# Kernel optimization log

Measured on AMD Instinct MI355X. Metric: run time of the kernel, lower is better.

The kernel has to match this reference:

```python
import jax, jax.numpy as jnp
import numpy as np

N_NODES = 50000


def _gcn_conv(x, edge_index, W, b):
    # x: [N, F_in], edge_index: [2, E] (with self-loops already added)
    n = x.shape[0]
    src, dst = edge_index[0], edge_index[1]
    h = x @ W  # [N, F_out] transform first (as in PyG GCNConv)
    deg = jax.ops.segment_sum(jnp.ones_like(dst, dtype=h.dtype), dst, num_segments=n)
    dinv = jax.lax.rsqrt(jnp.maximum(deg, 1.0))  # self-loops guarantee deg >= 1
    norm = dinv[src] * dinv[dst]  # [E]
    msg = h[src] * norm[:, None]  # [E, F_out] gather + scale
    out = jax.ops.segment_sum(msg, dst, num_segments=n)  # scatter-add to targets
    return out + b


def setup_inputs() -> dict:
    key = jax.random.key(0)
    k1, k2, k3, k4 = jax.random.split(key, 4)
    num_features, hidden, num_classes = 128, 128, 16
    n, e = N_NODES, 800000
    x = jax.random.normal(k1, (n, num_features), dtype=jnp.float32)
    edge_index = jax.random.randint(k2, (2, e), 0, n, dtype=jnp.int64)
    # add self-loops (PyG GCNConv default add_self_loops=True)
    loops = jnp.arange(n, dtype=jnp.int64)
    edge_index = jnp.concatenate([edge_index, jnp.stack([loops, loops])], axis=1)
    s1 = 1.0 / np.sqrt(num_features)
    s2 = 1.0 / np.sqrt(hidden)
    W1 = jax.random.uniform(k3, (num_features, hidden), jnp.float32, -s1, s1)
    b1 = jnp.zeros((hidden,), jnp.float32)
    W2 = jax.random.uniform(k4, (hidden, num_classes), jnp.float32, -s2, s2)
    b2 = jnp.zeros((num_classes,), jnp.float32)
    return {"x": x, "edge_index": edge_index, "W1": W1, "b1": b1, "W2": W2, "b2": b2}


def reference(x, edge_index, W1, b1, W2, b2):
    h = jax.nn.relu(_gcn_conv(x, edge_index, W1, b1))
    # dropout is identity in eval mode (deterministic reference)
    h = _gcn_conv(h, edge_index, W2, b2)
    return jax.nn.log_softmax(h, axis=1)
```

## Files before the change

kernel.cpp:

```cpp
#include <hip/hip_runtime.h>


typedef unsigned int uint32;
typedef unsigned short u16;
typedef __attribute__((ext_vector_type(8))) short bf16x8;
typedef __attribute__((ext_vector_type(4))) float f32x4;

#define NBMAX 1024
#define CHUNK 4096
#define EH 8192

__device__ inline u16 bf16rn(float f) {
    unsigned u = __float_as_uint(f);
    return (u16)((u + 0x7fffu + ((u >> 16) & 1u)) >> 16);
}

__device__ inline void bffma(float2& a, float w, uint32 u) {
    a.x = fmaf(w, __uint_as_float(u << 16), a.x);
    a.y = fmaf(w, __uint_as_float(u & 0xffff0000u), a.y);
}

__global__ __launch_bounds__(256) void k_combo(
    const float* __restrict__ x, const float* __restrict__ W1,
    const int* __restrict__ dstv, int* __restrict__ gh,
    u16* __restrict__ h, int N, int E, int NB, int ntile)
{
    __shared__ __align__(16) unsigned char smem[128 * 136 * 2];
    int t = threadIdx.x;

    if ((int)blockIdx.x >= ntile) {
        int* hl = (int*)smem;
        int hb = blockIdx.x - ntile;
        int e0 = hb * EH, e1 = min(e0 + EH, E);
        for (int i = t; i < NB; i += 256) hl[i] = 0;
        __syncthreads();
        for (int e = e0 + t; e < e1; e += 256)
            atomicAdd(&hl[dstv[e] >> 8], 1);
        __syncthreads();
        for (int i = t; i < NB; i += 256) {
            int c = hl[i];
            if (c) atomicAdd(&gh[i], c);
        }
        return;
    }

    u16* Wl = (u16*)smem;
    const float4* Wg4 = (const float4*)W1;
    for (int g = t; g < 128 * 32; g += 256) {
        int k = g >> 5, n4 = (g & 31) * 4;
        float4 v = Wg4[g];
        Wl[(n4 + 0) * 136 + k] = bf16rn(v.x);
        Wl[(n4 + 1) * 136 + k] = bf16rn(v.y);
        Wl[(n4 + 2) * 136 + k] = bf16rn(v.z);
        Wl[(n4 + 3) * 136 + k] = bf16rn(v.w);
    }
    __syncthreads();

    int wave = t >> 6, lane = t & 63;
    int quad = lane >> 4, ln = lane & 15;
    int rowbase = blockIdx.x * 64 + wave * 16;
    int node = rowbase + ln;
    int rclamp = min(node, N - 1);

    f32x4 acc[8];
    #pragma unroll
    for (int ct = 0; ct < 8; ++ct) acc[ct] = (f32x4){0.f, 0.f, 0.f, 0.f};

    #pragma unroll
    for (int q = 0; q < 4; ++q) {
        const float4* xr = (const float4*)(x + (size_t)rclamp * 128 + q * 32 + quad * 8);
        float4 a0 = xr[0], a1 = xr[1];
        bf16x8 xfr;
        xfr[0] = (short)bf16rn(a0.x); xfr[1] = (short)bf16rn(a0.y);
        xfr[2] = (short)bf16rn(a0.z); xfr[3] = (short)bf16rn(a0.w);
        xfr[4] = (short)bf16rn(a1.x); xfr[5] = (short)bf16rn(a1.y);
        xfr[6] = (short)bf16rn(a1.z); xfr[7] = (short)bf16rn(a1.w);
        #pragma unroll
        for (int ct = 0; ct < 8; ++ct) {
            bf16x8 wfr = *(const bf16x8*)&Wl[(ct * 16 + ln) * 136 + q * 32 + quad * 8];
            acc[ct] = __builtin_amdgcn_mfma_f32_16x16x32_bf16(wfr, xfr, acc[ct], 0, 0, 0);
        }
    }
    if (node < N) {
        u16* hp = h + (size_t)node * 128 + quad * 4;
        #pragma unroll
        for (int ct = 0; ct < 8; ++ct) {
            uint2 v;
            v.x = (uint32)bf16rn(acc[ct][0]) | ((uint32)bf16rn(acc[ct][1]) << 16);
            v.y = (uint32)bf16rn(acc[ct][2]) | ((uint32)bf16rn(acc[ct][3]) << 16);
            *(uint2*)(hp + ct * 16) = v;
        }
    }
}

__global__ __launch_bounds__(1024) void k_scanB(
    const int* __restrict__ gh, int* __restrict__ bbase,
    int* __restrict__ bfill, int NB, int E)
{
    __shared__ int s[1024];
    int t = threadIdx.x;
    int v = (t < NB) ? gh[t] : 0;
    s[t] = v;
    __syncthreads();
    for (int off = 1; off < 1024; off <<= 1) {
        int u = (t >= off) ? s[t - off] : 0;
        __syncthreads();
        s[t] += u;
        __syncthreads();
    }
    if (t < NB) {
        bbase[t] = s[t] - v;
        bfill[t] = 0;
    }
    if (t == 0) bbase[NB] = E;
}

__global__ __launch_bounds__(512) void k_partition(
    const int* __restrict__ src, const int* __restrict__ dstv,
    const int* __restrict__ bbase, int* __restrict__ bfill,
    uint32* __restrict__ tmp, int E, int NB)
{
    __shared__ int cntL[NBMAX];
    __shared__ int baseL[NBMAX];
    int t = threadIdx.x;
    int e0 = blockIdx.x * CHUNK;
    int e1 = min(e0 + CHUNK, E);
    for (int i = t; i < NB; i += 512) cntL[i] = 0;
    __syncthreads();
    for (int e = e0 + t; e < e1; e += 512)
        atomicAdd(&cntL[dstv[e] >> 8], 1);
    __syncthreads();
    for (int i = t; i < NB; i += 512) {
        int cc = cntL[i];
        baseL[i] = cc ? bbase[i] + atomicAdd(&bfill[i], cc) : 0;
        cntL[i] = 0;
    }
    __syncthreads();
    for (int e = e0 + t; e < e1; e += 512) {
        int sv = src[e], d = dstv[e];
        int b = d >> 8;
        int r = atomicAdd(&cntL[b], 1);
        tmp[baseL[b] + r] = (uint32)sv | ((uint32)(d & 255) << 16);
    }
}

__global__ __launch_bounds__(512) void k_bsort(
    const uint32* __restrict__ tmp, const int* __restrict__ bbase,
    u16* __restrict__ ssrc, int* __restrict__ rs,
    float* __restrict__ dinv, int N)
{
    __shared__ int cnt[256];
    __shared__ int ofs[256];
    int t = threadIdx.x;
    int b = blockIdx.x;
    int base = bbase[b];
    int endb = bbase[b + 1];
    int node0 = b << 8;

    if (t < 256) cnt[t] = 0;
    __syncthreads();
    for (int i = base + t; i < endb; i += 512)
        atomicAdd(&cnt[(tmp[i] >> 16) & 255], 1);
    __syncthreads();
    int v = (t < 256) ? cnt[t] : 0;
    __syncthreads();
    for (int off = 1; off < 256; off <<= 1) {
        int u = (t >= off && t < 256) ? cnt[t - off] : 0;
        __syncthreads();
        if (t < 256) cnt[t] += u;
        __syncthreads();
    }
    if (t < 256) {
        int node = node0 + t;
        if (node < N) {
            dinv[node] = rsqrtf(fmaxf((float)v, 1.0f));
            rs[node] = base + cnt[t];
        }
        ofs[t] = base + cnt[t] - v;
    }
    __syncthreads();
    for (int i = base + t; i < endb; i += 512) {
        uint32 rec = tmp[i];
        int pos = atomicAdd(&ofs[(rec >> 16) & 255], 1);
        ssrc[pos] = (u16)(rec & 0xffffu);
    }
}

__global__ __launch_bounds__(256) void k_pullg(
    const int* __restrict__ rs, const u16* __restrict__ ssrc,
    const float* __restrict__ dinv, const uint2* __restrict__ h,
    const float* __restrict__ b1, const float* __restrict__ W2,
    u16* __restrict__ h2, int N)
{
    __shared__ float W2T[16 * 132];
    __shared__ float rowbuf[8 * 132];
    int t = threadIdx.x;

    for (int g = t; g < 2048; g += 256) {
        int k = g >> 4, f = g & 15;
        W2T[f * 132 + k] = W2[g];
    }

    int wave = t >> 6, lane = t & 63;
    int sub = lane >> 5;
    int rl = lane & 31;
    int rowbase = blockIdx.x * 8;
    int n = rowbase + wave * 2 + sub;
    bool valid = (n < N);
    int nc = valid ? n : 0;
    int start = valid ? ((nc == 0) ? 0 : rs[nc - 1]) : 0;
    int len   = valid ? (rs[nc] - start) : 0;
    float dn  = valid ? dinv[nc] : 0.f;
    int lenMax = max(len, __shfl_xor(len, 32));

    float2 aA[4], aB[4];
    #pragma unroll
    for (int k = 0; k < 4; ++k) {
        aA[k] = (float2){0.f, 0.f};
        aB[k] = (float2){0.f, 0.f};
    }

    for (int tt = 0; tt < lenMax; tt += 4) {
        int s[4];
        uint2 u[4];
        float w[4];
        #pragma unroll
        for (int k = 0; k < 4; ++k) {
            bool act = (tt + k) < len;
            int jj = act ? (start + tt + k) : 0;
            s[k] = (int)ssrc[jj];
            w[k] = act ? 1.f : 0.f;
        }
        #pragma unroll
        for (int k = 0; k < 4; ++k)
            u[k] = h[(size_t)s[k] * 32 + rl];
        #pragma unroll
        for (int k = 0; k < 4; ++k)
            w[k] *= dn * dinv[s[k]];
        #pragma unroll
        for (int k = 0; k < 4; ++k) {
            bffma(aA[k], w[k], u[k].x);
            bffma(aB[k], w[k], u[k].y);
        }
    }

    {
        int r = wave * 2 + sub;
        float4 bb = ((const float4*)b1)[rl];
        float4 v;
        v.x = fmaxf(((aA[0].x + aA[1].x) + (aA[2].x + aA[3].x)) + bb.x, 0.f);
        v.y = fmaxf(((aA[0].y + aA[1].y) + (aA[2].y + aA[3].y)) + bb.y, 0.f);
        v.z = fmaxf(((aB[0].x + aB[1].x) + (aB[2].x + aB[3].x)) + bb.z, 0.f);
        v.w = fmaxf(((aB[0].y + aB[1].y) + (aB[2].y + aB[3].y)) + bb.w, 0.f);
        ((float4*)rowbuf)[r * 33 + rl] = v;
    }
    __syncthreads();

    if (t < 128) {
        int f = t & 15, r = t >> 4;
        const float4* W4 = (const float4*)W2T;
        const float4* rb4 = (const float4*)rowbuf;
        float acc = 0.f;
        #pragma unroll 8
        for (int k4 = 0; k4 < 32; ++k4) {
            float4 w = W4[f * 33 + k4];
            float4 xv = rb4[r * 33 + k4];
            acc = fmaf(xv.x, w.x, acc);
            acc = fmaf(xv.y, w.y, acc);
            acc = fmaf(xv.z, w.z, acc);
            acc = fmaf(xv.w, w.w, acc);
        }
        int rn = rowbase + r;
        if (rn < N) h2[(size_t)rn * 16 + f] = bf16rn(acc);
    }
}

__global__ __launch_bounds__(256) void k_pull2(
    const int* __restrict__ rs, const u16* __restrict__ ssrc,
    const float* __restrict__ dinv, const uint32* __restrict__ h2,
    const float* __restrict__ b2, float* __restrict__ out, int N)
{
    int idx = blockIdx.x * 256 + threadIdx.x;
    int n = idx >> 3;
    if (n >= N) return;
    int c = idx & 7;
    int start = (n == 0) ? 0 : rs[n - 1];
    int len = rs[n] - start;
    float dn = dinv[n];

    float2 a[4];
    #pragma unroll
    for (int k = 0; k < 4; ++k) a[k] = (float2){0.f, 0.f};

    for (int tt = 0; tt < len; tt += 4) {
        int s[4];
        uint32 u[4];
        float w[4];
        #pragma unroll
        for (int k = 0; k < 4; ++k) {
            bool act = (tt + k) < len;
            int jj = act ? (start + tt + k) : 0;
            s[k] = (int)ssrc[jj];
            w[k] = act ? 1.f : 0.f;
        }
        #pragma unroll
        for (int k = 0; k < 4; ++k)
            u[k] = h2[(size_t)s[k] * 8 + c];
        #pragma unroll
        for (int k = 0; k < 4; ++k)
            w[k] *= dn * dinv[s[k]];
        #pragma unroll
        for (int k = 0; k < 4; ++k)
            bffma(a[k], w[k], u[k]);
    }

    float acc0 = (a[0].x + a[1].x) + (a[2].x + a[3].x);
    float acc1 = (a[0].y + a[1].y) + (a[2].y + a[3].y);
    float v0 = acc0 + b2[2 * c];
    float v1 = acc1 + b2[2 * c + 1];
    float m = fmaxf(v0, v1);
    #pragma unroll
    for (int off = 1; off < 8; off <<= 1) m = fmaxf(m, __shfl_xor(m, off));
    float s = expf(v0 - m) + expf(v1 - m);
    #pragma unroll
    for (int off = 1; off < 8; off <<= 1) s += __shfl_xor(s, off);
    float ls = logf(s);
    float2 r = {v0 - m - ls, v1 - m - ls};
    ((float2*)out)[(size_t)n * 8 + c] = r;
}

extern "C" void kernel_launch(void* const* d_in, const int* in_sizes, int n_in,
                              void* d_out, int out_size, void* d_ws, size_t ws_size,
                              hipStream_t stream) {
    const float* x  = (const float*)d_in[0];
    const int*   ei = (const int*)d_in[1];
    const float* W1 = (const float*)d_in[2];
    const float* b1 = (const float*)d_in[3];
    const float* W2 = (const float*)d_in[4];
    const float* b2 = (const float*)d_in[5];
    float* outp = (float*)d_out;

    const int E = in_sizes[1] / 2;
    const int N = in_sizes[0] / 128;
    const int NB = (N + 255) >> 8;
    const int NH = (E + EH - 1) / EH;
    const int ntile = (N + 63) / 64;
    const int* src  = ei;
    const int* dstv = ei + E;

    const int Npad = (N + 255) & ~255;
    const int Epad = (E + 255) & ~255;
    int*   gh    = (int*)d_ws;
    int*   bbase = gh + NBMAX;
    int*   bfill = bbase + NBMAX + 256;
    int*   rs    = bfill + NBMAX;
    float* dinv  = (float*)(rs + Npad);
    uint32* tmp  = (uint32*)(dinv + Npad);
    u16*   ssrc  = (u16*)(tmp + Epad);
    uintptr_t hp = ((uintptr_t)(ssrc + Epad) + 255) & ~(uintptr_t)255;
    u16*   h     = (u16*)hp;
    u16*   h2    = h + (size_t)Npad * 128;

    hipMemsetAsync(gh, 0, NBMAX * sizeof(int), stream);
    k_combo<<<ntile + NH, 256, 0, stream>>>(x, W1, dstv, gh, h, N, E, NB, ntile);
    k_scanB<<<1, 1024, 0, stream>>>(gh, bbase, bfill, NB, E);
    k_partition<<<(E + CHUNK - 1) / CHUNK, 512, 0, stream>>>(src, dstv, bbase,
                                                             bfill, tmp, E, NB);
    k_bsort<<<NB, 512, 0, stream>>>(tmp, bbase, ssrc, rs, dinv, N);
    k_pullg<<<(N + 7) / 8, 256, 0, stream>>>(rs, ssrc, dinv, (const uint2*)h,
                                             b1, W2, h2, N);
    k_pull2<<<(N * 8 + 255) / 256, 256, 0, stream>>>(rs, ssrc, dinv,
                                                     (const uint32*)h2, b2, outp, N);
}
```

Baseline: 172.1 us.

## Tune partition/bsort sizes, wave-shuffle scan, deeper unrolled gather in layer-1 pull

Halves the partition chunk size so more blocks share the work, and doubles the bsort block size to 1024 threads. The block-wide scan now uses wavefront shuffles plus a small cross-wave pass instead of a barrier-heavy shared-memory Hillis-Steele loop. The layer-1 gather loop issues 8 neighbour loads per iteration instead of 4 for more memory-level parallelism, and the destination normalisation is moved out of the loop into a single final multiply. The larger unroll raises register pressure, and the smaller chunk adds more global atomics on the bucket fill counters.

```diff
diff --git a/kernel.cpp b/kernel.cpp
--- a/kernel.cpp
+++ b/kernel.cpp
@@ -7,7 +7,7 @@
 typedef __attribute__((ext_vector_type(4))) float f32x4;
 
 #define NBMAX 1024
-#define CHUNK 4096
+#define CHUNK 2048
 #define EH 8192
 
 __device__ inline u16 bf16rn(float f) {
@@ -97,19 +97,32 @@
     const int* __restrict__ gh, int* __restrict__ bbase,
     int* __restrict__ bfill, int NB, int E)
 {
-    __shared__ int s[1024];
-    int t = threadIdx.x;
+    __shared__ int wsum[16];
+    int t = threadIdx.x;
+    int lane = t & 63, wv = t >> 6;
     int v = (t < NB) ? gh[t] : 0;
-    s[t] = v;
-    __syncthreads();
-    for (int off = 1; off < 1024; off <<= 1) {
-        int u = (t >= off) ? s[t - off] : 0;
-        __syncthreads();
-        s[t] += u;
-        __syncthreads();
-    }
+    int sc = v;
+    #pragma unroll
+    for (int off = 1; off < 64; off <<= 1) {
+        int u = __shfl_up(sc, off);
+        if (lane >= off) sc += u;
+    }
+    if (lane == 63) wsum[wv] = sc;
+    __syncthreads();
+    if (wv == 0 && lane < 16) {
+        int b = wsum[lane];
+        int bs = b;
+        #pragma unroll
+        for (int off = 1; off < 16; off <<= 1) {
+            int u = __shfl_up(bs, off);
+            if (lane >= off) bs += u;
+        }
+        wsum[lane] = bs - b;
+    }
+    __syncthreads();
+    int incl = sc + wsum[wv];
     if (t < NB) {
-        bbase[t] = s[t] - v;
+        bbase[t] = incl - v;
         bfill[t] = 0;
     }
     if (t == 0) bbase[NB] = E;
@@ -144,7 +157,7 @@
     }
 }
 
-__global__ __launch_bounds__(512) void k_bsort(
+__global__ __launch_bounds__(1024) void k_bsort(
     const uint32* __restrict__ tmp, const int* __restrict__ bbase,
     u16* __restrict__ ssrc, int* __restrict__ rs,
     float* __restrict__ dinv, int N)
@@ -159,7 +172,7 @@
 
     if (t < 256) cnt[t] = 0;
     __syncthreads();
-    for (int i = base + t; i < endb; i += 512)
+    for (int i = base + t; i < endb; i += 1024)
         atomicAdd(&cnt[(tmp[i] >> 16) & 255], 1);
     __syncthreads();
     int v = (t < 256) ? cnt[t] : 0;
@@ -179,7 +192,7 @@
         ofs[t] = base + cnt[t] - v;
     }
     __syncthreads();
-    for (int i = base + t; i < endb; i += 512) {
+    for (int i = base + t; i < endb; i += 1024) {
         uint32 rec = tmp[i];
         int pos = atomicAdd(&ofs[(rec >> 16) & 255], 1);
         ssrc[pos] = (u16)(rec & 0xffffu);
@@ -220,27 +233,27 @@
         aB[k] = (float2){0.f, 0.f};
     }
 
-    for (int tt = 0; tt < lenMax; tt += 4) {
-        int s[4];
-        uint2 u[4];
-        float w[4];
-        #pragma unroll
-        for (int k = 0; k < 4; ++k) {
+    for (int tt = 0; tt < lenMax; tt += 8) {
+        int s[8];
+        uint2 u[8];
+        float w[8];
+        #pragma unroll
+        for (int k = 0; k < 8; ++k) {
             bool act = (tt + k) < len;
             int jj = act ? (start + tt + k) : 0;
             s[k] = (int)ssrc[jj];
             w[k] = act ? 1.f : 0.f;
         }
         #pragma unroll
-        for (int k = 0; k < 4; ++k)
+        for (int k = 0; k < 8; ++k)
             u[k] = h[(size_t)s[k] * 32 + rl];
         #pragma unroll
-        for (int k = 0; k < 4; ++k)
-            w[k] *= dn * dinv[s[k]];
-        #pragma unroll
-        for (int k = 0; k < 4; ++k) {
-            bffma(aA[k], w[k], u[k].x);
-            bffma(aB[k], w[k], u[k].y);
+        for (int k = 0; k < 8; ++k)
+            w[k] *= dinv[s[k]];
+        #pragma unroll
+        for (int k = 0; k < 8; ++k) {
+            bffma(aA[k & 3], w[k], u[k].x);
+            bffma(aB[k & 3], w[k], u[k].y);
         }
     }
 
@@ -248,10 +261,10 @@
         int r = wave * 2 + sub;
         float4 bb = ((const float4*)b1)[rl];
         float4 v;
-        v.x = fmaxf(((aA[0].x + aA[1].x) + (aA[2].x + aA[3].x)) + bb.x, 0.f);
-        v.y = fmaxf(((aA[0].y + aA[1].y) + (aA[2].y + aA[3].y)) + bb.y, 0.f);
-        v.z = fmaxf(((aB[0].x + aB[1].x) + (aB[2].x + aB[3].x)) + bb.z, 0.f);
-        v.w = fmaxf(((aB[0].y + aB[1].y) + (aB[2].y + aB[3].y)) + bb.w, 0.f);
+        v.x = fmaxf(fmaf(dn, (aA[0].x + aA[1].x) + (aA[2].x + aA[3].x), bb.x), 0.f);
+        v.y = fmaxf(fmaf(dn, (aA[0].y + aA[1].y) + (aA[2].y + aA[3].y), bb.y), 0.f);
+        v.z = fmaxf(fmaf(dn, (aB[0].x + aB[1].x) + (aB[2].x + aB[3].x), bb.z), 0.f);
+        v.w = fmaxf(fmaf(dn, (aB[0].y + aB[1].y) + (aB[2].y + aB[3].y), bb.w), 0.f);
         ((float4*)rowbuf)[r * 33 + rl] = v;
     }
     __syncthreads();
@@ -366,7 +379,7 @@
     k_scanB<<<1, 1024, 0, stream>>>(gh, bbase, bfill, NB, E);
     k_partition<<<(E + CHUNK - 1) / CHUNK, 512, 0, stream>>>(src, dstv, bbase,
                                                              bfill, tmp, E, NB);
-    k_bsort<<<NB, 512, 0, stream>>>(tmp, bbase, ssrc, rs, dinv, N);
+    k_bsort<<<NB, 1024, 0, stream>>>(tmp, bbase, ssrc, rs, dinv, N);
     k_pullg<<<(N + 7) / 8, 256, 0, stream>>>(rs, ssrc, dinv, (const uint2*)h,
                                              b1, W2, h2, N);
     k_pull2<<<(N * 8 + 255) / 256, 256, 0, stream>>>(rs, ssrc, dinv,
```

After: 172.1 us. About the same (-0.0%).
